# Optimization experiments

Measured on AMD Instinct MI355X. Metric: run time of the kernel, lower is better.

Reference implementation:

```python
import jax, jax.numpy as jnp
import numpy as np

B, S, H = 8, 256, 128
LA, LR = 2, 2
L = LA + LR
HD = H // L  # head_size = 32
SCALE = 1.0 / np.sqrt(HD).astype(np.float32)


def setup_inputs() -> dict:
    key = jax.random.key(0)
    ks = jax.random.split(key, 16)
    w = 0.02
    return {
        'hidden_states': jax.random.normal(ks[0], (B, S, H), jnp.float32),
        'attention_mask': jnp.zeros((B, 1, S, S), jnp.float32),
        'abs0': jax.random.normal(ks[1], (B, S, H), jnp.float32),
        'abs1': jax.random.normal(ks[2], (B, S, H), jnp.float32),
        'rel0': jax.random.normal(ks[3], (B, S, S, H), jnp.float32),
        'rel1': jax.random.normal(ks[4], (B, S, S, H), jnp.float32),
        'Wq': jax.random.normal(ks[5], (H, H), jnp.float32) * w,
        'bq': jnp.zeros((H,), jnp.float32),
        'Wk': jax.random.normal(ks[6], (H, H), jnp.float32) * w,
        'bk': jnp.zeros((H,), jnp.float32),
        'Wv': jax.random.normal(ks[7], (H, H), jnp.float32) * w,
        'bv': jnp.zeros((H,), jnp.float32),
        'Wo': jax.random.normal(ks[8], (H, H), jnp.float32) * w,
        'bo': jnp.zeros((H,), jnp.float32),
    }


def reference(hidden_states, attention_mask, abs0, abs1, rel0, rel1,
              Wq, bq, Wk, bk, Wv, bv, Wo, bo):
    # Projections; heads dim is L (= La+Lr), head size HD
    Q = (hidden_states @ Wq + bq).reshape(B, S, L, HD).transpose(0, 2, 1, 3)  # [B,L,S,HD]
    K = (hidden_states @ Wk + bk).reshape(B, S, L, HD).transpose(0, 2, 1, 3)
    V = (hidden_states @ Wv + bv).reshape(B, S, L, HD).transpose(0, 2, 1, 3)

    scores = jnp.einsum('blqh,blkh->blqk', Q, K) * SCALE  # [B,L,S,S]

    # Absolute-kernel heads 0..La-1: key-project only head i's slice of Wk
    for i, ae in enumerate((abs0, abs1)):
        aK = ae @ Wk[:, i * HD:(i + 1) * HD] + bk[i * HD:(i + 1) * HD]  # [B,S,HD]
        scores = scores.at[:, i].add(jnp.einsum('bqh,bkh->bqk', Q[:, i], aK) * SCALE)

    # Relative-kernel heads La..L-1: per-(q,k) relative key slice
    for i, re in enumerate((rel0, rel1)):
        h = LA + i
        rK = re @ Wk[:, h * HD:(h + 1) * HD] + bk[h * HD:(h + 1) * HD]  # [B,S,S,HD]
        scores = scores.at[:, h].add(jnp.einsum('bqh,bqkh->bqk', Q[:, h], rK) * SCALE)

    scores = scores + attention_mask
    probs = jax.nn.softmax(scores, axis=-1)  # [B,L,S,S]

    ctx = jnp.einsum('blqk,blkh->blqh', probs, V)  # [B,L,S,HD]

    for i, ae in enumerate((abs0, abs1)):
        aV = ae @ Wv[:, i * HD:(i + 1) * HD] + bv[i * HD:(i + 1) * HD]  # [B,S,HD]
        ctx = ctx.at[:, i].add(jnp.einsum('bqk,bkh->bqh', probs[:, i], aV))

    for i, re in enumerate((rel0, rel1)):
        h = LA + i
        rV = re @ Wv[:, h * HD:(h + 1) * HD] + bv[h * HD:(h + 1) * HD]  # [B,S,S,HD]
        ctx = ctx.at[:, h].add(jnp.einsum('bqk,bqkh->bqh', probs[:, h], rV))

    ctx = ctx.transpose(0, 2, 1, 3).reshape(B, S, H)
    return ctx @ Wo + bo
```

## Files before the change

### kernel.cpp

```cpp
#include <hip/hip_runtime.h>

#define Bc 8
#define Sc 256
#define Hc 128
#define HDc 32
#define NHc 4
#define SCALE 0.17677669529663687f

__global__ __launch_bounds__(256) void mmha_kernel(
    const float* __restrict__ hs,
    const float* __restrict__ am,
    const float* __restrict__ abs0,
    const float* __restrict__ abs1,
    const float* __restrict__ rel0,
    const float* __restrict__ rel1,
    const float* __restrict__ Wq, const float* __restrict__ bq,
    const float* __restrict__ Wk, const float* __restrict__ bk,
    const float* __restrict__ Wv, const float* __restrict__ bv,
    const float* __restrict__ Wo, const float* __restrict__ bo,
    float* __restrict__ out)
{
    const int t = threadIdx.x;
    const int bqi = blockIdx.x;
    const int b = bqi >> 8;
    const int q = bqi & 255;

    __shared__ float hsrow[Hc];
    __shared__ float Qrow[Hc];
    __shared__ float qk_sh[NHc * Hc];
    __shared__ float cb_sh[NHc];
    __shared__ float mask_row[Sc];
    __shared__ float4 red4[256];
    __shared__ float l_sh[8];
    __shared__ float rbarn[Hc];
    __shared__ float ctx_sh[Hc];

    const size_t rowbase = (size_t)(b * Sc + q) * Hc;

    if (t < Hc) hsrow[t] = hs[rowbase + t];
    mask_row[t] = am[((size_t)(b * Sc) + q) * Sc + t];
    __syncthreads();

    if (t < Hc) {
        float acc = bq[t];
        #pragma unroll 16
        for (int c = 0; c < Hc; ++c) acc += hsrow[c] * Wq[c * Hc + t];
        Qrow[t] = acc;
    }
    __syncthreads();

    if (t < Hc) {
        float pv = Qrow[t] * bk[t];
        #pragma unroll
        for (int off = 16; off >= 1; off >>= 1) pv += __shfl_xor(pv, off, 32);
        if ((t & 31) == 0) cb_sh[t >> 5] = 2.0f * pv;
    }
    for (int rep = 0; rep < 2; ++rep) {
        int idx = rep * 256 + t;
        int h = idx >> 7, cp = idx & 127;
        const float4* wkr = (const float4*)(Wk + cp * Hc + h * HDc);
        const float4* qr  = (const float4*)(Qrow + h * HDc);
        float acc = 0.f;
        #pragma unroll
        for (int j = 0; j < HDc / 4; ++j) {
            float4 wv = wkr[j];
            float4 qv = qr[j];
            acc += wv.x * qv.x + wv.y * qv.y + wv.z * qv.z + wv.w * qv.w;
        }
        qk_sh[h * Hc + cp] = acc;
    }
    __syncthreads();

    const int c4 = t & 31;
    const int part = t >> 5;
    const float4* hs4 = (const float4*)(hs + (size_t)b * Sc * Hc);

    for (int h = 0; h < NHc; ++h) {
        const float* eb;
        if (h == 0)      eb = abs0 + (size_t)b * Sc * Hc;
        else if (h == 1) eb = abs1 + (size_t)b * Sc * Hc;
        else if (h == 2) eb = rel0 + (size_t)(b * Sc + q) * Sc * Hc;
        else             eb = rel1 + (size_t)(b * Sc + q) * Sc * Hc;
        const float4* e4 = (const float4*)eb;

        const float4 qreg = ((const float4*)(qk_sh + h * Hc))[c4];
        const float cb = cb_sh[h];

        float4 acc; acc.x = acc.y = acc.z = acc.w = 0.f;
        float l = 0.f;

        #pragma unroll 4
        for (int r = 0; r < 32; ++r) {
            const int row = r * 8 + part;
            const size_t off = (size_t)row * (Hc / 4) + c4;
            const float4 a = hs4[off];
            const float4 e = e4[off];
            float4 v;
            v.x = a.x + e.x; v.y = a.y + e.y;
            v.z = a.z + e.z; v.w = a.w + e.w;
            float pv = v.x * qreg.x + v.y * qreg.y + v.z * qreg.z + v.w * qreg.w;
            #pragma unroll
            for (int off2 = 16; off2 >= 1; off2 >>= 1) pv += __shfl_xor(pv, off2, 32);
            const float p = __expf((pv + cb) * SCALE + mask_row[row]);
            l += p;
            acc.x += p * v.x; acc.y += p * v.y;
            acc.z += p * v.z; acc.w += p * v.w;
        }

        red4[t] = acc;
        if (c4 == 0) l_sh[part] = l;
        __syncthreads();
        if (t < 32) {
            float4 tot; tot.x = tot.y = tot.z = tot.w = 0.f;
            #pragma unroll
            for (int g = 0; g < 8; ++g) {
                float4 v = red4[g * 32 + t];
                tot.x += v.x; tot.y += v.y; tot.z += v.z; tot.w += v.w;
            }
            float lt = 0.f;
            #pragma unroll
            for (int g = 0; g < 8; ++g) lt += l_sh[g];
            const float inv = 1.0f / lt;
            float4 r; r.x = tot.x * inv; r.y = tot.y * inv;
                      r.z = tot.z * inv; r.w = tot.w * inv;
            ((float4*)rbarn)[t] = r;
        }
        __syncthreads();
        if (t < 32) {
            float cv = 2.0f * bv[h * HDc + t];
            #pragma unroll 8
            for (int c = 0; c < Hc; ++c) cv += rbarn[c] * Wv[c * Hc + h * HDc + t];
            ctx_sh[h * HDc + t] = cv;
        }
        __syncthreads();
    }

    if (t < Hc) {
        float ov = bo[t];
        #pragma unroll 16
        for (int c = 0; c < Hc; ++c) ov += ctx_sh[c] * Wo[c * Hc + t];
        out[rowbase + t] = ov;
    }
}

extern "C" void kernel_launch(void* const* d_in, const int* in_sizes, int n_in,
                              void* d_out, int out_size, void* d_ws, size_t ws_size,
                              hipStream_t stream) {
    const float* hs = (const float*)d_in[0];
    const float* am = (const float*)d_in[1];
    const float* a0 = (const float*)d_in[2];
    const float* a1 = (const float*)d_in[3];
    const float* r0 = (const float*)d_in[4];
    const float* r1 = (const float*)d_in[5];
    const float* Wq = (const float*)d_in[6];
    const float* bq = (const float*)d_in[7];
    const float* Wk = (const float*)d_in[8];
    const float* bk = (const float*)d_in[9];
    const float* Wv = (const float*)d_in[10];
    const float* bv = (const float*)d_in[11];
    const float* Wo = (const float*)d_in[12];
    const float* bo = (const float*)d_in[13];

    mmha_kernel<<<dim3(Bc * Sc), dim3(256), 0, stream>>>(
        hs, am, a0, a1, r0, r1, Wq, bq, Wk, bk, Wv, bv, Wo, bo, (float*)d_out);
}
```

Measured before the change: 612.0 us.

## Process all four heads in one streaming pass and batch the Wv projection

Fuses the four per-head loops into a single loop over rows that loads the hidden-state row once and issues all four embedding loads together. This cuts the redundant hs reloads and puts more memory requests in flight per iteration. The per-head Wv projection, which used only 32 threads, is replaced by one 128-thread pass over per-head padded shared buffers. A launch-bounds occupancy hint is also added. The cost is higher register use for four accumulators, which the occupancy hint may force into spills.

```diff
diff --git a/kernel.cpp b/kernel.cpp
--- a/kernel.cpp
+++ b/kernel.cpp
@@ -7,7 +7,7 @@
 #define NHc 4
 #define SCALE 0.17677669529663687f
 
-__global__ __launch_bounds__(256) void mmha_kernel(
+__global__ __launch_bounds__(256, 4) void mmha_kernel(
     const float* __restrict__ hs,
     const float* __restrict__ am,
     const float* __restrict__ abs0,
@@ -32,7 +32,7 @@
     __shared__ float mask_row[Sc];
     __shared__ float4 red4[256];
     __shared__ float l_sh[8];
-    __shared__ float rbarn[Hc];
+    __shared__ float rbarn[NHc * 132];
     __shared__ float ctx_sh[Hc];
 
     const size_t rowbase = (size_t)(b * Sc + q) * Hc;
@@ -73,42 +73,57 @@
 
     const int c4 = t & 31;
     const int part = t >> 5;
-    const float4* hs4 = (const float4*)(hs + (size_t)b * Sc * Hc);
 
+    const float4* hs4 = (const float4*)(hs)   + (size_t)b * Sc * (Hc / 4);
+    const float4* e0p = (const float4*)(abs0) + (size_t)b * Sc * (Hc / 4);
+    const float4* e1p = (const float4*)(abs1) + (size_t)b * Sc * (Hc / 4);
+    const float4* e2p = (const float4*)(rel0) + (size_t)(b * Sc + q) * Sc * (Hc / 4);
+    const float4* e3p = (const float4*)(rel1) + (size_t)(b * Sc + q) * Sc * (Hc / 4);
+
+    float4 qreg[NHc];
+    float  cbr[NHc];
+    float4 acc[NHc];
+    float  l[NHc];
+    #pragma unroll
     for (int h = 0; h < NHc; ++h) {
-        const float* eb;
-        if (h == 0)      eb = abs0 + (size_t)b * Sc * Hc;
-        else if (h == 1) eb = abs1 + (size_t)b * Sc * Hc;
-        else if (h == 2) eb = rel0 + (size_t)(b * Sc + q) * Sc * Hc;
-        else             eb = rel1 + (size_t)(b * Sc + q) * Sc * Hc;
-        const float4* e4 = (const float4*)eb;
+        qreg[h] = ((const float4*)(qk_sh + h * Hc))[c4];
+        cbr[h]  = cb_sh[h];
+        acc[h].x = acc[h].y = acc[h].z = acc[h].w = 0.f;
+        l[h] = 0.f;
+    }
 
-        const float4 qreg = ((const float4*)(qk_sh + h * Hc))[c4];
-        const float cb = cb_sh[h];
+    #pragma unroll 2
+    for (int r = 0; r < 32; ++r) {
+        const int row = r * 8 + part;
+        const int off = row * (Hc / 4) + c4;
+        const float4 a = hs4[off];
+        float4 e[NHc];
+        e[0] = e0p[off];
+        e[1] = e1p[off];
+        e[2] = e2p[off];
+        e[3] = e3p[off];
+        const float m = mask_row[row];
+        #pragma unroll
+        for (int h = 0; h < NHc; ++h) {
+            float4 v;
+            v.x = a.x + e[h].x; v.y = a.y + e[h].y;
+            v.z = a.z + e[h].z; v.w = a.w + e[h].w;
+            float pv = v.x * qreg[h].x + v.y * qreg[h].y
+                     + v.z * qreg[h].z + v.w * qreg[h].w;
+            #pragma unroll
+            for (int o = 16; o >= 1; o >>= 1) pv += __shfl_xor(pv, o, 32);
+            const float p = __expf((pv + cbr[h]) * SCALE + m);
+            l[h] += p;
+            acc[h].x += p * v.x; acc[h].y += p * v.y;
+            acc[h].z += p * v.z; acc[h].w += p * v.w;
+        }
+    }
 
-        float4 acc; acc.x = acc.y = acc.z = acc.w = 0.f;
-        float l = 0.f;
-
-        #pragma unroll 4
-        for (int r = 0; r < 32; ++r) {
-            const int row = r * 8 + part;
-            const size_t off = (size_t)row * (Hc / 4) + c4;
-            const float4 a = hs4[off];
-            const float4 e = e4[off];
-            float4 v;
-            v.x = a.x + e.x; v.y = a.y + e.y;
-            v.z = a.z + e.z; v.w = a.w + e.w;
-            float pv = v.x * qreg.x + v.y * qreg.y + v.z * qreg.z + v.w * qreg.w;
-            #pragma unroll
-            for (int off2 = 16; off2 >= 1; off2 >>= 1) pv += __shfl_xor(pv, off2, 32);
-            const float p = __expf((pv + cb) * SCALE + mask_row[row]);
-            l += p;
-            acc.x += p * v.x; acc.y += p * v.y;
-            acc.z += p * v.z; acc.w += p * v.w;
-        }
-
-        red4[t] = acc;
-        if (c4 == 0) l_sh[part] = l;
+    #pragma unroll
+    for (int h = 0; h < NHc; ++h) {
+        __syncthreads();
+        red4[t] = acc[h];
+        if (c4 == 0) l_sh[part] = l[h];
         __syncthreads();
         if (t < 32) {
             float4 tot; tot.x = tot.y = tot.z = tot.w = 0.f;
@@ -121,19 +136,21 @@
             #pragma unroll
             for (int g = 0; g < 8; ++g) lt += l_sh[g];
             const float inv = 1.0f / lt;
-            float4 r; r.x = tot.x * inv; r.y = tot.y * inv;
-                      r.z = tot.z * inv; r.w = tot.w * inv;
-            ((float4*)rbarn)[t] = r;
+            float4 rv; rv.x = tot.x * inv; rv.y = tot.y * inv;
+                       rv.z = tot.z * inv; rv.w = tot.w * inv;
+            ((float4*)(rbarn + h * 132))[t] = rv;
         }
-        __syncthreads();
-        if (t < 32) {
-            float cv = 2.0f * bv[h * HDc + t];
-            #pragma unroll 8
-            for (int c = 0; c < Hc; ++c) cv += rbarn[c] * Wv[c * Hc + h * HDc + t];
-            ctx_sh[h * HDc + t] = cv;
-        }
-        __syncthreads();
     }
+    __syncthreads();
+
+    if (t < Hc) {
+        const float* rb = rbarn + (t >> 5) * 132;
+        float cv = 2.0f * bv[t];
+        #pragma unroll 8
+        for (int c = 0; c < Hc; ++c) cv += rb[c] * Wv[c * Hc + t];
+        ctx_sh[t] = cv;
+    }
+    __syncthreads();
 
     if (t < Hc) {
         float ov = bo[t];
```

Result: faster. 596.7 us (-2.5%).
